# Kernel tuning notes

Hardware: AMD Instinct MI355X
Metric: run time of the kernel (lower is better)

## Reference

```python
import jax, jax.numpy as jnp
import numpy as np

B, D, H, C, T, F = 4096, 1024, 2048, 1000, 819200, 32


def setup_inputs() -> dict:
    key = jax.random.key(0)
    ks = jax.random.split(key, 12)
    feature_vector = jax.random.normal(ks[0], (B, D), dtype=jnp.float32)
    var_flat = jax.random.normal(ks[1], (T, F), dtype=jnp.float32)
    segment_ids = jnp.sort(jax.random.randint(ks[2], (T,), 0, B))
    target_vector = jax.random.randint(ks[3], (B,), 0, C)
    target_scalar = jax.random.normal(ks[4], (B,), dtype=jnp.float32)
    # learned params (torch Linear convention: W [out, in])
    Wv = jax.random.normal(ks[5], (D, F), dtype=jnp.float32) / np.sqrt(F)
    bv = jnp.zeros((D,), dtype=jnp.float32)
    W1 = jax.random.normal(ks[6], (H, D), dtype=jnp.float32) / np.sqrt(D)
    b1 = jnp.zeros((H,), dtype=jnp.float32)
    W2 = jax.random.normal(ks[7], (C, H), dtype=jnp.float32) / np.sqrt(H)
    b2 = jnp.zeros((C,), dtype=jnp.float32)
    Ws = jax.random.normal(ks[8], (1, H), dtype=jnp.float32) / np.sqrt(H)
    bs = jnp.zeros((1,), dtype=jnp.float32)
    return {
        "feature_vector": feature_vector, "var_flat": var_flat,
        "segment_ids": segment_ids, "target_vector": target_vector,
        "target_scalar": target_scalar, "Wv": Wv, "bv": bv,
        "W1": W1, "b1": b1, "W2": W2, "b2": b2, "Ws": Ws, "bs": bs,
    }


def reference(feature_vector, var_flat, segment_ids, target_vector, target_scalar,
              Wv, bv, W1, b1, W2, b2, Ws, bs):
    nb = feature_vector.shape[0]
    # ragged per-item mean via segment reduce (replaces python loop)
    sums = jax.ops.segment_sum(var_flat, segment_ids, num_segments=nb)      # [B, 32]
    counts = jax.ops.segment_sum(jnp.ones((var_flat.shape[0],), var_flat.dtype),
                                 segment_ids, num_segments=nb)
    means = sums / jnp.maximum(counts, 1.0)[:, None]
    var_processed = means @ Wv.T + bv                                        # [B, D]
    combined = feature_vector + var_processed
    hidden = jax.nn.relu(combined @ W1.T + b1)                               # [B, H]
    vector_output = hidden @ W2.T + b2                                       # [B, C]
    scalar_output = (hidden @ Ws.T + bs).squeeze(-1)                         # [B]
    logp = jax.nn.log_softmax(vector_output, axis=-1)
    loss_vector = -jnp.mean(jnp.take_along_axis(logp, target_vector[:, None], axis=1))
    loss_scalar = jnp.mean(jnp.square(scalar_output - target_scalar))
    total_loss = loss_vector + loss_scalar
    acc = jnp.mean((jnp.argmax(vector_output, axis=1) == target_vector).astype(jnp.float32))
    return total_loss, loss_vector, loss_scalar, acc
```

## Files before the change

kernel.cpp:

```cpp
#include <hip/hip_runtime.h>
#include <hip/hip_bf16.h>
#include <math.h>

#define B_  4096
#define D_  1024
#define H_  2048
#define C_  1000
#define T_  819200
#define F_  32
#define NPAD2 1024
#define NPART 1024

typedef __attribute__((ext_vector_type(8))) short short8;
typedef __attribute__((ext_vector_type(4))) float f32x4;

static const size_t WS_SUMS     = 0;
static const size_t WS_COUNTS   = WS_SUMS + (size_t)B_ * F_ * 4;
static const size_t WS_ZERO_SZ  = WS_COUNTS + (size_t)B_ * 4;
static const size_t WS_PV       = WS_ZERO_SZ;
static const size_t WS_PA       = WS_PV + NPART * 4;
static const size_t WS_PS       = WS_PA + NPART * 4;
static const size_t WS_COMBINED = 1u << 20;
static const size_t WS_W1BF     = WS_COMBINED + (size_t)B_ * D_ * 2;
static const size_t WS_W2BF     = WS_W1BF + (size_t)H_ * D_ * 2;
static const size_t WS_HIDDEN   = WS_W2BF + (size_t)NPAD2 * H_ * 2;
static const size_t WS_LOGITS   = WS_HIDDEN + (size_t)B_ * H_ * 2;

#define RPT 32
__global__ __launch_bounds__(256) void seg_reduce_kernel(
    const float* __restrict__ var_flat, const int* __restrict__ seg_ids,
    float* __restrict__ sums, float* __restrict__ counts) {
  int gt  = blockIdx.x * 256 + threadIdx.x;
  int c4  = (gt & 7) * 4;
  long base = (long)(gt >> 3) * RPT;
  int cur = -1;
  float a0 = 0.f, a1 = 0.f, a2 = 0.f, a3 = 0.f, cnt = 0.f;
  for (int r = 0; r < RPT; ++r) {
    long row = base + r;
    int s = seg_ids[row];
    float4 v = *(const float4*)(var_flat + row * F_ + c4);
    if (s != cur) {
      if (cur >= 0) {
        float* dst = &sums[(size_t)cur * F_ + c4];
        atomicAdd(dst + 0, a0); atomicAdd(dst + 1, a1);
        atomicAdd(dst + 2, a2); atomicAdd(dst + 3, a3);
        if (c4 == 0) atomicAdd(&counts[cur], cnt);
      }
      cur = s; a0 = a1 = a2 = a3 = 0.f; cnt = 0.f;
    }
    a0 += v.x; a1 += v.y; a2 += v.z; a3 += v.w; cnt += 1.f;
  }
  if (cur >= 0) {
    float* dst = &sums[(size_t)cur * F_ + c4];
    atomicAdd(dst + 0, a0); atomicAdd(dst + 1, a1);
    atomicAdd(dst + 2, a2); atomicAdd(dst + 3, a3);
    if (c4 == 0) atomicAdd(&counts[cur], cnt);
  }
}

__global__ __launch_bounds__(256) void cvt_bf16_kernel(
    const float* __restrict__ src, __hip_bfloat16* __restrict__ dst, int n8) {
  int i = blockIdx.x * 256 + threadIdx.x;
  if (i >= n8) return;
  size_t off = (size_t)i * 8;
  float4 a = *(const float4*)(src + off);
  float4 b = *(const float4*)(src + off + 4);
  __hip_bfloat16 t[8];
  t[0] = __float2bfloat16(a.x); t[1] = __float2bfloat16(a.y);
  t[2] = __float2bfloat16(a.z); t[3] = __float2bfloat16(a.w);
  t[4] = __float2bfloat16(b.x); t[5] = __float2bfloat16(b.y);
  t[6] = __float2bfloat16(b.z); t[7] = __float2bfloat16(b.w);
  *(uint4*)(dst + off) = *(uint4*)t;
}

__global__ __launch_bounds__(256) void cvt_w2_kernel(
    const float* __restrict__ src, __hip_bfloat16* __restrict__ dst) {
  int i = blockIdx.x * 256 + threadIdx.x;
  size_t off = (size_t)i * 8;
  int row = (int)(off / H_);
  __hip_bfloat16 t[8];
  if (row < C_) {
    float4 a = *(const float4*)(src + off);
    float4 b = *(const float4*)(src + off + 4);
    t[0] = __float2bfloat16(a.x); t[1] = __float2bfloat16(a.y);
    t[2] = __float2bfloat16(a.z); t[3] = __float2bfloat16(a.w);
    t[4] = __float2bfloat16(b.x); t[5] = __float2bfloat16(b.y);
    t[6] = __float2bfloat16(b.z); t[7] = __float2bfloat16(b.w);
  } else {
    for (int e = 0; e < 8; ++e) t[e] = __float2bfloat16(0.f);
  }
  *(uint4*)(dst + off) = *(uint4*)t;
}

__global__ __launch_bounds__(256) void combined_kernel(
    const float* __restrict__ feat, const float* __restrict__ sums,
    const float* __restrict__ counts, const float* __restrict__ Wv,
    const float* __restrict__ bv, __hip_bfloat16* __restrict__ combined) {
  __shared__ float m[8][F_];
  int b0  = blockIdx.y * 8;
  int tid = threadIdx.x;
  {
    int seg = tid >> 5, col = tid & 31;
    float c = counts[b0 + seg];
    c = c < 1.f ? 1.f : c;
    m[seg][col] = sums[(size_t)(b0 + seg) * F_ + col] / c;
  }
  __syncthreads();
  int d = blockIdx.x * 256 + tid;
  float w[F_];
  {
    const float4* wv = (const float4*)(Wv + (size_t)d * F_);
#pragma unroll
    for (int f4 = 0; f4 < F_ / 4; ++f4) {
      float4 x = wv[f4];
      w[f4 * 4 + 0] = x.x; w[f4 * 4 + 1] = x.y;
      w[f4 * 4 + 2] = x.z; w[f4 * 4 + 3] = x.w;
    }
  }
  float bvd = bv[d];
#pragma unroll
  for (int bb = 0; bb < 8; ++bb) {
    float acc = feat[(size_t)(b0 + bb) * D_ + d] + bvd;
#pragma unroll
    for (int f = 0; f < F_; ++f) acc = fmaf(m[bb][f], w[f], acc);
    combined[(size_t)(b0 + bb) * D_ + d] = __float2bfloat16(acc);
  }
}

__device__ inline void load16_lds(const short* g, short* l) {
  __builtin_amdgcn_global_load_lds(
      (const __attribute__((address_space(1))) void*)g,
      (__attribute__((address_space(3))) void*)l, 16, 0, 0);
}

template <int MODE>
__global__ __launch_bounds__(256) void gemm_mfma_kernel(
    const short* __restrict__ A, const short* __restrict__ Bm,
    const float* __restrict__ bias, void* __restrict__ Cout,
    int M, int K, int Nout) {
  __shared__ short As[4096];
  __shared__ short Bs[4096];
  const int tid  = threadIdx.x;
  const int lane = tid & 63;
  const int w    = tid >> 6;
  const int bm = blockIdx.y * 128;
  const int bn = blockIdx.x * 128;
  const int wm = (w >> 1) * 64;
  const int wn = (w & 1) * 64;
  const int m_lane = lane & 15;
  const int quad   = lane >> 4;

  f32x4 acc[4][4];
#pragma unroll
  for (int i = 0; i < 4; ++i)
#pragma unroll
    for (int j = 0; j < 4; ++j) acc[i][j] = f32x4{0.f, 0.f, 0.f, 0.f};

  const int c0 = w * 128 + lane;
  const int c1 = c0 + 64;
  const short* gA0 = A + (size_t)(bm + (c0 & 127)) * K + (c0 >> 7) * 8;
  const short* gA1 = A + (size_t)(bm + (c1 & 127)) * K + (c1 >> 7) * 8;
  const short* gB0 = Bm + (size_t)(bn + (c0 & 127)) * K + (c0 >> 7) * 8;
  const short* gB1 = Bm + (size_t)(bn + (c1 & 127)) * K + (c1 >> 7) * 8;
  short* lA0 = As + (size_t)w * 1024;
  short* lA1 = lA0 + 512;
  short* lB0 = Bs + (size_t)w * 1024;
  short* lB1 = lB0 + 512;

  for (int k0 = 0; k0 < K; k0 += 32) {
    __syncthreads();
    load16_lds(gA0 + k0, lA0);
    load16_lds(gA1 + k0, lA1);
    load16_lds(gB0 + k0, lB0);
    load16_lds(gB1 + k0, lB1);
    __syncthreads();
    short8 af[4], bf[4];
#pragma unroll
    for (int i = 0; i < 4; ++i)
      af[i] = *(const short8*)&As[quad * 1024 + (wm + i * 16 + m_lane) * 8];
#pragma unroll
    for (int j = 0; j < 4; ++j)
      bf[j] = *(const short8*)&Bs[quad * 1024 + (wn + j * 16 + m_lane) * 8];
#pragma unroll
    for (int i = 0; i < 4; ++i)
#pragma unroll
      for (int j = 0; j < 4; ++j)
        acc[i][j] = __builtin_amdgcn_mfma_f32_16x16x32_bf16(af[i], bf[j], acc[i][j], 0, 0, 0);
  }

  const int row0 = bm + wm + quad * 4;
  const int col0 = bn + wn + m_lane;
  if (MODE == 0) {
    __hip_bfloat16* Cb = (__hip_bfloat16*)Cout;
#pragma unroll
    for (int j = 0; j < 4; ++j) {
      int col = col0 + j * 16;
      float bsv = bias[col];
#pragma unroll
      for (int i = 0; i < 4; ++i)
#pragma unroll
        for (int r = 0; r < 4; ++r) {
          int row = row0 + i * 16 + r;
          float v = acc[i][j][r] + bsv;
          v = v > 0.f ? v : 0.f;
          Cb[(size_t)row * Nout + col] = __float2bfloat16(v);
        }
    }
  } else {
    float* Cf = (float*)Cout;
#pragma unroll
    for (int j = 0; j < 4; ++j) {
      int col = col0 + j * 16;
      if (col < Nout) {
        float bsv = bias[col];
#pragma unroll
        for (int i = 0; i < 4; ++i)
#pragma unroll
          for (int r = 0; r < 4; ++r) {
            int row = row0 + i * 16 + r;
            Cf[(size_t)row * Nout + col] = acc[i][j][r] + bsv;
          }
      }
    }
  }
}

__global__ __launch_bounds__(256) void scalar_loss_kernel(
    const __hip_bfloat16* __restrict__ hidden, const float* __restrict__ Ws,
    const float* __restrict__ bs, const float* __restrict__ tgt,
    float* __restrict__ ps) {
  int tid  = threadIdx.x;
  int lane = tid & 63;
  int w    = tid >> 6;
  int b    = blockIdx.x * 4 + w;
  const uint4*  h4 = (const uint4*)(hidden + (size_t)b * H_);
  const float4* w4 = (const float4*)Ws;
  float s = 0.f;
#pragma unroll
  for (int k = 0; k < 4; ++k) {
    int ch = lane + 64 * k;
    uint4 p = h4[ch];
    float4 w0 = w4[2 * ch], w1 = w4[2 * ch + 1];
    float a0 = __uint_as_float(p.x << 16), a1 = __uint_as_float(p.x & 0xffff0000u);
    float a2 = __uint_as_float(p.y << 16), a3 = __uint_as_float(p.y & 0xffff0000u);
    float a4 = __uint_as_float(p.z << 16), a5 = __uint_as_float(p.z & 0xffff0000u);
    float a6 = __uint_as_float(p.w << 16), a7 = __uint_as_float(p.w & 0xffff0000u);
    s += a0 * w0.x + a1 * w0.y + a2 * w0.z + a3 * w0.w +
         a4 * w1.x + a5 * w1.y + a6 * w1.z + a7 * w1.w;
  }
#pragma unroll
  for (int o = 32; o > 0; o >>= 1) s += __shfl_down(s, o, 64);
  __shared__ float sq[4];
  if (lane == 0) {
    float d = s + bs[0] - tgt[b];
    sq[w] = d * d;
  }
  __syncthreads();
  if (tid == 0) ps[blockIdx.x] = sq[0] + sq[1] + sq[2] + sq[3];
}

__global__ __launch_bounds__(256) void softmax_loss_kernel(
    const float* __restrict__ logits, const int* __restrict__ target,
    float* __restrict__ pv, float* __restrict__ pa) {
  int tid  = threadIdx.x;
  int lane = tid & 63;
  int w    = tid >> 6;
  int b    = blockIdx.x * 4 + w;
  const float*  row  = logits + (size_t)b * C_;
  const float4* row4 = (const float4*)row;
  const int C4 = C_ / 4;
  float v[16];
  float vmax = -INFINITY;
  int   imax = 0x7fffffff;
#pragma unroll
  for (int k = 0; k < 4; ++k) {
    int c4 = lane + 64 * k;
    float4 x = (c4 < C4) ? row4[c4]
                         : make_float4(-INFINITY, -INFINITY, -INFINITY, -INFINITY);
    v[k * 4 + 0] = x.x; v[k * 4 + 1] = x.y; v[k * 4 + 2] = x.z; v[k * 4 + 3] = x.w;
#pragma unroll
    for (int e = 0; e < 4; ++e) {
      float val = v[k * 4 + e];
      int   idx = c4 * 4 + e;
      if (val > vmax) { vmax = val; imax = idx; }
    }
  }
#pragma unroll
  for (int o = 32; o > 0; o >>= 1) {
    float ov = __shfl_down(vmax, o, 64);
    int   oi = __shfl_down(imax, o, 64);
    if (ov > vmax || (ov == vmax && oi < imax)) { vmax = ov; imax = oi; }
  }
  vmax = __shfl(vmax, 0, 64);
  float se = 0.f;
#pragma unroll
  for (int j = 0; j < 16; ++j) se += expf(v[j] - vmax);
#pragma unroll
  for (int o = 32; o > 0; o >>= 1) se += __shfl_down(se, o, 64);
  __shared__ float s_nll[4];
  __shared__ float s_acc[4];
  if (lane == 0) {
    int t = target[b];
    float logp = row[t] - vmax - logf(se);
    s_nll[w] = -logp;
    s_acc[w] = (imax == t) ? 1.f : 0.f;
  }
  __syncthreads();
  if (tid == 0) {
    pv[blockIdx.x] = s_nll[0] + s_nll[1] + s_nll[2] + s_nll[3];
    pa[blockIdx.x] = s_acc[0] + s_acc[1] + s_acc[2] + s_acc[3];
  }
}

__global__ __launch_bounds__(256) void finalize_kernel(
    const float* __restrict__ pv, const float* __restrict__ pa,
    const float* __restrict__ ps, float* __restrict__ out) {
  int tid  = threadIdx.x;
  int lane = tid & 63;
  int w    = tid >> 6;
  float nll = 0.f, acc = 0.f, sq = 0.f;
  for (int i = tid; i < NPART; i += 256) {
    nll += pv[i]; acc += pa[i]; sq += ps[i];
  }
#pragma unroll
  for (int o = 32; o > 0; o >>= 1) {
    nll += __shfl_down(nll, o, 64);
    acc += __shfl_down(acc, o, 64);
    sq  += __shfl_down(sq,  o, 64);
  }
  __shared__ float sn[4], sa[4], ss[4];
  if (lane == 0) { sn[w] = nll; sa[w] = acc; ss[w] = sq; }
  __syncthreads();
  if (tid == 0) {
    float lv = (sn[0] + sn[1] + sn[2] + sn[3]) * (1.f / B_);
    float ls = (ss[0] + ss[1] + ss[2] + ss[3]) * (1.f / B_);
    float ac = (sa[0] + sa[1] + sa[2] + sa[3]) * (1.f / B_);
    out[0] = lv + ls;
    out[1] = lv;
    out[2] = ls;
    out[3] = ac;
  }
}

extern "C" void kernel_launch(void* const* d_in, const int* in_sizes, int n_in,
                              void* d_out, int out_size, void* d_ws, size_t ws_size,
                              hipStream_t stream) {
  const float* feature  = (const float*)d_in[0];
  const float* var_flat = (const float*)d_in[1];
  const int*   seg_ids  = (const int*)d_in[2];
  const int*   tgt_vec  = (const int*)d_in[3];
  const float* tgt_scal = (const float*)d_in[4];
  const float* Wv = (const float*)d_in[5];
  const float* bv = (const float*)d_in[6];
  const float* W1 = (const float*)d_in[7];
  const float* b1 = (const float*)d_in[8];
  const float* W2 = (const float*)d_in[9];
  const float* b2 = (const float*)d_in[10];
  const float* Ws = (const float*)d_in[11];
  const float* bs = (const float*)d_in[12];
  float* out = (float*)d_out;

  char* ws = (char*)d_ws;
  float* sums   = (float*)(ws + WS_SUMS);
  float* counts = (float*)(ws + WS_COUNTS);
  float* pv     = (float*)(ws + WS_PV);
  float* pa     = (float*)(ws + WS_PA);
  float* ps     = (float*)(ws + WS_PS);
  __hip_bfloat16* combined_bf = (__hip_bfloat16*)(ws + WS_COMBINED);
  __hip_bfloat16* W1bf        = (__hip_bfloat16*)(ws + WS_W1BF);
  __hip_bfloat16* W2bf        = (__hip_bfloat16*)(ws + WS_W2BF);
  __hip_bfloat16* hidden_bf   = (__hip_bfloat16*)(ws + WS_HIDDEN);
  float*          logits      = (float*)(ws + WS_LOGITS);

  hipMemsetAsync(ws, 0, WS_ZERO_SZ, stream);

  seg_reduce_kernel<<<(T_ / RPT) * 8 / 256, 256, 0, stream>>>(var_flat, seg_ids, sums, counts);

  cvt_bf16_kernel<<<(H_ * D_ / 8 + 255) / 256, 256, 0, stream>>>(W1, W1bf, H_ * D_ / 8);
  cvt_w2_kernel<<<(NPAD2 * H_ / 8) / 256, 256, 0, stream>>>(W2, W2bf);

  {
    dim3 grid(D_ / 256, B_ / 8);
    combined_kernel<<<grid, 256, 0, stream>>>(feature, sums, counts, Wv, bv, combined_bf);
  }

  {
    dim3 grid(H_ / 128, B_ / 128);
    gemm_mfma_kernel<0><<<grid, 256, 0, stream>>>(
        (const short*)combined_bf, (const short*)W1bf, b1, hidden_bf, B_, D_, H_);
  }

  {
    dim3 grid(NPAD2 / 128, B_ / 128);
    gemm_mfma_kernel<1><<<grid, 256, 0, stream>>>(
        (const short*)hidden_bf, (const short*)W2bf, b2, logits, B_, H_, C_);
  }

  scalar_loss_kernel<<<B_ / 4, 256, 0, stream>>>(hidden_bf, Ws, bs, tgt_scal, ps);

  softmax_loss_kernel<<<B_ / 4, 256, 0, stream>>>(logits, tgt_vec, pv, pa);

  finalize_kernel<<<1, 256, 0, stream>>>(pv, pa, ps, out);
}
```

Measured before the change: 351.3 us.

## Double-buffer GEMM LDS tiles and fold scalar head into padded W2 GEMM

The MFMA GEMM gets two LDS buffers so the next K-slice's global-to-LDS loads are issued before the current slice is computed, and one barrier per iteration is removed. The scalar head Ws is packed into the zero padding row C of the bf16 W2 matrix, with a padded bias vector, so the second GEMM produces the scalar output as an extra logit column. The separate scalar-loss pass over hidden is removed and merged with the softmax loss into one kernel. The cost is double the LDS per block, a bf16-rounded Ws, and an extra tiny bias-padding kernel.

```diff
diff --git a/kernel.cpp b/kernel.cpp
--- a/kernel.cpp
+++ b/kernel.cpp
@@ -20,6 +20,7 @@
 static const size_t WS_PV       = WS_ZERO_SZ;
 static const size_t WS_PA       = WS_PV + NPART * 4;
 static const size_t WS_PS       = WS_PA + NPART * 4;
+static const size_t WS_B2P      = WS_PS + NPART * 4;
 static const size_t WS_COMBINED = 1u << 20;
 static const size_t WS_W1BF     = WS_COMBINED + (size_t)B_ * D_ * 2;
 static const size_t WS_W2BF     = WS_W1BF + (size_t)H_ * D_ * 2;
@@ -74,14 +75,18 @@
 }
 
 __global__ __launch_bounds__(256) void cvt_w2_kernel(
-    const float* __restrict__ src, __hip_bfloat16* __restrict__ dst) {
+    const float* __restrict__ W2, const float* __restrict__ Ws,
+    __hip_bfloat16* __restrict__ dst) {
   int i = blockIdx.x * 256 + threadIdx.x;
   size_t off = (size_t)i * 8;
   int row = (int)(off / H_);
   __hip_bfloat16 t[8];
-  if (row < C_) {
-    float4 a = *(const float4*)(src + off);
-    float4 b = *(const float4*)(src + off + 4);
+  const float* src = nullptr;
+  if (row < C_)       src = W2 + off;
+  else if (row == C_) src = Ws + (off - (size_t)C_ * H_);
+  if (src) {
+    float4 a = *(const float4*)(src);
+    float4 b = *(const float4*)(src + 4);
     t[0] = __float2bfloat16(a.x); t[1] = __float2bfloat16(a.y);
     t[2] = __float2bfloat16(a.z); t[3] = __float2bfloat16(a.w);
     t[4] = __float2bfloat16(b.x); t[5] = __float2bfloat16(b.y);
@@ -90,6 +95,16 @@
     for (int e = 0; e < 8; ++e) t[e] = __float2bfloat16(0.f);
   }
   *(uint4*)(dst + off) = *(uint4*)t;
+}
+
+__global__ __launch_bounds__(256) void pad_bias_kernel(
+    const float* __restrict__ b2, const float* __restrict__ bs,
+    float* __restrict__ b2p) {
+  int i = blockIdx.x * 256 + threadIdx.x;
+  float v = 0.f;
+  if (i < C_) v = b2[i];
+  else if (i == C_) v = bs[0];
+  b2p[i] = v;
 }
 
 __global__ __launch_bounds__(256) void combined_kernel(
@@ -138,8 +153,8 @@
     const short* __restrict__ A, const short* __restrict__ Bm,
     const float* __restrict__ bias, void* __restrict__ Cout,
     int M, int K, int Nout) {
-  __shared__ short As[4096];
-  __shared__ short Bs[4096];
+  __shared__ short As[2][4096];
+  __shared__ short Bs[2][4096];
   const int tid  = threadIdx.x;
   const int lane = tid & 63;
   const int w    = tid >> 6;
@@ -162,25 +177,32 @@
   const short* gA1 = A + (size_t)(bm + (c1 & 127)) * K + (c1 >> 7) * 8;
   const short* gB0 = Bm + (size_t)(bn + (c0 & 127)) * K + (c0 >> 7) * 8;
   const short* gB1 = Bm + (size_t)(bn + (c1 & 127)) * K + (c1 >> 7) * 8;
-  short* lA0 = As + (size_t)w * 1024;
-  short* lA1 = lA0 + 512;
-  short* lB0 = Bs + (size_t)w * 1024;
-  short* lB1 = lB0 + 512;
-
-  for (int k0 = 0; k0 < K; k0 += 32) {
+  const int l0 = w * 1024;
+  const int l1 = l0 + 512;
+
+  load16_lds(gA0, &As[0][l0]);
+  load16_lds(gA1, &As[0][l1]);
+  load16_lds(gB0, &Bs[0][l0]);
+  load16_lds(gB1, &Bs[0][l1]);
+
+  const int iters = K >> 5;
+  for (int it = 0; it < iters; ++it) {
+    const int cur = it & 1, nxt = cur ^ 1;
     __syncthreads();
-    load16_lds(gA0 + k0, lA0);
-    load16_lds(gA1 + k0, lA1);
-    load16_lds(gB0 + k0, lB0);
-    load16_lds(gB1 + k0, lB1);
-    __syncthreads();
+    const int k1 = (it + 1) << 5;
+    if (k1 < K) {
+      load16_lds(gA0 + k1, &As[nxt][l0]);
+      load16_lds(gA1 + k1, &As[nxt][l1]);
+      load16_lds(gB0 + k1, &Bs[nxt][l0]);
+      load16_lds(gB1 + k1, &Bs[nxt][l1]);
+    }
     short8 af[4], bf[4];
 #pragma unroll
     for (int i = 0; i < 4; ++i)
-      af[i] = *(const short8*)&As[quad * 1024 + (wm + i * 16 + m_lane) * 8];
+      af[i] = *(const short8*)&As[cur][quad * 1024 + (wm + i * 16 + m_lane) * 8];
 #pragma unroll
     for (int j = 0; j < 4; ++j)
-      bf[j] = *(const short8*)&Bs[quad * 1024 + (wn + j * 16 + m_lane) * 8];
+      bf[j] = *(const short8*)&Bs[cur][quad * 1024 + (wn + j * 16 + m_lane) * 8];
 #pragma unroll
     for (int i = 0; i < 4; ++i)
 #pragma unroll
@@ -211,79 +233,46 @@
 #pragma unroll
     for (int j = 0; j < 4; ++j) {
       int col = col0 + j * 16;
-      if (col < Nout) {
-        float bsv = bias[col];
-#pragma unroll
-        for (int i = 0; i < 4; ++i)
-#pragma unroll
-          for (int r = 0; r < 4; ++r) {
-            int row = row0 + i * 16 + r;
-            Cf[(size_t)row * Nout + col] = acc[i][j][r] + bsv;
-          }
-      }
-    }
-  }
-}
-
-__global__ __launch_bounds__(256) void scalar_loss_kernel(
-    const __hip_bfloat16* __restrict__ hidden, const float* __restrict__ Ws,
-    const float* __restrict__ bs, const float* __restrict__ tgt,
-    float* __restrict__ ps) {
+      float bsv = bias[col];
+#pragma unroll
+      for (int i = 0; i < 4; ++i)
+#pragma unroll
+        for (int r = 0; r < 4; ++r) {
+          int row = row0 + i * 16 + r;
+          Cf[(size_t)row * Nout + col] = acc[i][j][r] + bsv;
+        }
+    }
+  }
+}
+
+__global__ __launch_bounds__(256) void loss_kernel(
+    const float* __restrict__ logits, const int* __restrict__ target,
+    const float* __restrict__ tgt_scal,
+    float* __restrict__ pv, float* __restrict__ pa, float* __restrict__ ps) {
   int tid  = threadIdx.x;
   int lane = tid & 63;
   int w    = tid >> 6;
   int b    = blockIdx.x * 4 + w;
-  const uint4*  h4 = (const uint4*)(hidden + (size_t)b * H_);
-  const float4* w4 = (const float4*)Ws;
-  float s = 0.f;
-#pragma unroll
-  for (int k = 0; k < 4; ++k) {
-    int ch = lane + 64 * k;
-    uint4 p = h4[ch];
-    float4 w0 = w4[2 * ch], w1 = w4[2 * ch + 1];
-    float a0 = __uint_as_float(p.x << 16), a1 = __uint_as_float(p.x & 0xffff0000u);
-    float a2 = __uint_as_float(p.y << 16), a3 = __uint_as_float(p.y & 0xffff0000u);
-    float a4 = __uint_as_float(p.z << 16), a5 = __uint_as_float(p.z & 0xffff0000u);
-    float a6 = __uint_as_float(p.w << 16), a7 = __uint_as_float(p.w & 0xffff0000u);
-    s += a0 * w0.x + a1 * w0.y + a2 * w0.z + a3 * w0.w +
-         a4 * w1.x + a5 * w1.y + a6 * w1.z + a7 * w1.w;
-  }
-#pragma unroll
-  for (int o = 32; o > 0; o >>= 1) s += __shfl_down(s, o, 64);
-  __shared__ float sq[4];
-  if (lane == 0) {
-    float d = s + bs[0] - tgt[b];
-    sq[w] = d * d;
-  }
-  __syncthreads();
-  if (tid == 0) ps[blockIdx.x] = sq[0] + sq[1] + sq[2] + sq[3];
-}
-
-__global__ __launch_bounds__(256) void softmax_loss_kernel(
-    const float* __restrict__ logits, const int* __restrict__ target,
-    float* __restrict__ pv, float* __restrict__ pa) {
-  int tid  = threadIdx.x;
-  int lane = tid & 63;
-  int w    = tid >> 6;
-  int b    = blockIdx.x * 4 + w;
-  const float*  row  = logits + (size_t)b * C_;
+  const float*  row  = logits + (size_t)b * NPAD2;
   const float4* row4 = (const float4*)row;
-  const int C4 = C_ / 4;
   float v[16];
   float vmax = -INFINITY;
   int   imax = 0x7fffffff;
 #pragma unroll
   for (int k = 0; k < 4; ++k) {
     int c4 = lane + 64 * k;
-    float4 x = (c4 < C4) ? row4[c4]
-                         : make_float4(-INFINITY, -INFINITY, -INFINITY, -INFINITY);
-    v[k * 4 + 0] = x.x; v[k * 4 + 1] = x.y; v[k * 4 + 2] = x.z; v[k * 4 + 3] = x.w;
-#pragma unroll
-    for (int e = 0; e < 4; ++e) {
-      float val = v[k * 4 + e];
-      int   idx = c4 * 4 + e;
-      if (val > vmax) { vmax = val; imax = idx; }
-    }
+    float4 x = row4[c4];
+    float e0 = x.x, e1 = x.y, e2 = x.z, e3 = x.w;
+    int idx = c4 * 4;
+    if (idx + 0 >= C_) e0 = -INFINITY;
+    if (idx + 1 >= C_) e1 = -INFINITY;
+    if (idx + 2 >= C_) e2 = -INFINITY;
+    if (idx + 3 >= C_) e3 = -INFINITY;
+    v[k * 4 + 0] = e0; v[k * 4 + 1] = e1; v[k * 4 + 2] = e2; v[k * 4 + 3] = e3;
+    if (e0 > vmax) { vmax = e0; imax = idx + 0; }
+    if (e1 > vmax) { vmax = e1; imax = idx + 1; }
+    if (e2 > vmax) { vmax = e2; imax = idx + 2; }
+    if (e3 > vmax) { vmax = e3; imax = idx + 3; }
   }
 #pragma unroll
   for (int o = 32; o > 0; o >>= 1) {
@@ -297,18 +286,20 @@
   for (int j = 0; j < 16; ++j) se += expf(v[j] - vmax);
 #pragma unroll
   for (int o = 32; o > 0; o >>= 1) se += __shfl_down(se, o, 64);
-  __shared__ float s_nll[4];
-  __shared__ float s_acc[4];
+  __shared__ float s_nll[4], s_acc[4], s_sq[4];
   if (lane == 0) {
     int t = target[b];
     float logp = row[t] - vmax - logf(se);
     s_nll[w] = -logp;
     s_acc[w] = (imax == t) ? 1.f : 0.f;
+    float d = row[C_] - tgt_scal[b];
+    s_sq[w] = d * d;
   }
   __syncthreads();
   if (tid == 0) {
     pv[blockIdx.x] = s_nll[0] + s_nll[1] + s_nll[2] + s_nll[3];
     pa[blockIdx.x] = s_acc[0] + s_acc[1] + s_acc[2] + s_acc[3];
+    ps[blockIdx.x] = s_sq[0] + s_sq[1] + s_sq[2] + s_sq[3];
   }
 }
 
@@ -366,6 +357,7 @@
   float* pv     = (float*)(ws + WS_PV);
   float* pa     = (float*)(ws + WS_PA);
   float* ps     = (float*)(ws + WS_PS);
+  float* b2p    = (float*)(ws + WS_B2P);
   __hip_bfloat16* combined_bf = (__hip_bfloat16*)(ws + WS_COMBINED);
   __hip_bfloat16* W1bf        = (__hip_bfloat16*)(ws + WS_W1BF);
   __hip_bfloat16* W2bf        = (__hip_bfloat16*)(ws + WS_W2BF);
@@ -377,7 +369,8 @@
   seg_reduce_kernel<<<(T_ / RPT) * 8 / 256, 256, 0, stream>>>(var_flat, seg_ids, sums, counts);
 
   cvt_bf16_kernel<<<(H_ * D_ / 8 + 255) / 256, 256, 0, stream>>>(W1, W1bf, H_ * D_ / 8);
-  cvt_w2_kernel<<<(NPAD2 * H_ / 8) / 256, 256, 0, stream>>>(W2, W2bf);
+  cvt_w2_kernel<<<(NPAD2 * H_ / 8) / 256, 256, 0, stream>>>(W2, Ws, W2bf);
+  pad_bias_kernel<<<NPAD2 / 256, 256, 0, stream>>>(b2, bs, b2p);
 
   {
     dim3 grid(D_ / 256, B_ / 8);
@@ -393,12 +386,10 @@
   {
     dim3 grid(NPAD2 / 128, B_ / 128);
     gemm_mfma_kernel<1><<<grid, 256, 0, stream>>>(
-        (const short*)hidden_bf, (const short*)W2bf, b2, logits, B_, H_, C_);
-  }
-
-  scalar_loss_kernel<<<B_ / 4, 256, 0, stream>>>(hidden_bf, Ws, bs, tgt_scal, ps);
-
-  softmax_loss_kernel<<<B_ / 4, 256, 0, stream>>>(logits, tgt_vec, pv, pa);
+        (const short*)hidden_bf, (const short*)W2bf, b2p, logits, B_, H_, NPAD2);
+  }
+
+  loss_kernel<<<B_ / 4, 256, 0, stream>>>(logits, tgt_vec, tgt_scal, pv, pa, ps);
 
   finalize_kernel<<<1, 256, 0, stream>>>(pv, pa, ps, out);
 }
```

Measured after the change: 336.1 us. 1.05x faster.
